# Optimization experiments

Measured on AMD Instinct MI355X. Metric: run time of the kernel, lower is better.

Reference implementation:

```python
import jax, jax.numpy as jnp
import numpy as np

C_IN = 64
C_QK = C_IN // 8  # 8
B, H, W = 8, 64, 64


def setup_inputs() -> dict:
    key = jax.random.key(0)
    ks = jax.random.split(key, 8)
    s_in = 1.0 / np.sqrt(C_IN)
    return {
        "x": jax.random.normal(ks[0], (B, C_IN, H, W), dtype=jnp.float32),
        "Wf": jax.random.normal(ks[1], (C_QK, C_IN), dtype=jnp.float32) * s_in,
        "bf": jax.random.normal(ks[2], (C_QK,), dtype=jnp.float32) * 0.01,
        "Wg": jax.random.normal(ks[3], (C_QK, C_IN), dtype=jnp.float32) * s_in,
        "bg": jax.random.normal(ks[4], (C_QK,), dtype=jnp.float32) * 0.01,
        "Wh": jax.random.normal(ks[5], (C_IN, C_IN), dtype=jnp.float32) * s_in,
        "bh": jax.random.normal(ks[6], (C_IN,), dtype=jnp.float32) * 0.01,
        "gamma": jax.random.normal(ks[7], (1,), dtype=jnp.float32) * 0.1,
    }


def reference(x, Wf, bf, Wg, bg, Wh, bh, gamma):
    Bn, C, Hn, Wn = x.shape
    N = Hn * Wn
    xf = x.reshape(Bn, C, N)  # (B, C, HW)
    # 1x1 convs == per-pixel linear projections
    fx = jnp.einsum('bcn,oc->bno', xf, Wf) + bf            # (B, HW, C/8)  (permuted query)
    gx = jnp.einsum('bcn,oc->bon', xf, Wg) + bg[:, None]   # (B, C/8, HW)
    hx = jnp.einsum('bcn,oc->bon', xf, Wh) + bh[:, None]   # (B, C,  HW)
    s_mtx = jnp.einsum('bno,bom->bnm', fx, gx)             # (B, HW, HW)
    attention = jax.nn.softmax(s_mtx, axis=-2)             # softmax over dim=-2 (rows)
    o = jnp.einsum('bcn,bnm->bcm', hx, attention)          # (B, C, HW)
    return x + gamma * o.reshape(Bn, C, Hn, Wn)
```

## Files before the change

### kernel.cpp

```cpp
#include <hip/hip_runtime.h>
#include <hip/hip_bf16.h>
#include <math.h>

#define CIN 64
#define CQK 8
#define BATCH 8
#define NPOS 4096
#define TN 128
#define NT (NPOS / TN)

typedef __attribute__((ext_vector_type(8))) short s16x8;
typedef __attribute__((ext_vector_type(4))) float f32x4;
typedef __attribute__((ext_vector_type(16))) float f32x16;

#define Z16 {0,0,0,0,0,0,0,0,0,0,0,0,0,0,0,0}

__device__ inline unsigned cvt_pk_bf16(float lo, float hi) {
    unsigned r;
    asm("v_cvt_pk_bf16_f32 %0, %1, %2" : "=v"(r) : "v"(lo), "v"(hi));
    return r;
}

__global__ __launch_bounds__(256) void proj_kernel(
    const float* __restrict__ x,
    const float* __restrict__ Wf, const float* __restrict__ bf,
    const float* __restrict__ Wg, const float* __restrict__ bg,
    const float* __restrict__ Wh, const float* __restrict__ bh,
    unsigned short* __restrict__ Kp, unsigned short* __restrict__ Qp,
    unsigned short* __restrict__ Vimg)
{
    __shared__ float xs[CIN * 66];
    __shared__ float bss[80];

    const int tid = threadIdx.x;
    const int b   = blockIdx.y;
    const int n0  = blockIdx.x * 64;

    if (tid < 80)
        bss[tid] = (tid < 8) ? bf[tid] : (tid < 16) ? bg[tid - 8] : bh[tid - 16];

    {
        const int c   = tid >> 2;
        const int seg = tid & 3;
        const float* src = x + ((size_t)(b * CIN + c)) * NPOS + n0 + seg * 16;
        float* dst = xs + c * 66 + seg * 16;
#pragma unroll
        for (int k = 0; k < 4; ++k) {
            const float4 v = *(const float4*)(src + k * 4);
            *(float2*)(dst + k * 4)     = make_float2(v.x, v.y);
            *(float2*)(dst + k * 4 + 2) = make_float2(v.z, v.w);
        }
    }

    const int l  = tid & 63;
    const int w  = tid >> 6;
    const int lm = l & 15;
    const int h  = l >> 4;

    auto wfrag = [&](const float* Wrow) -> s16x8 {
        const float4 a  = *(const float4*)(Wrow);
        const float4 bq = *(const float4*)(Wrow + 4);
        union { unsigned u[4]; s16x8 v; } r;
        r.u[0] = cvt_pk_bf16(a.x, a.y);
        r.u[1] = cvt_pk_bf16(a.z, a.w);
        r.u[2] = cvt_pk_bf16(bq.x, bq.y);
        r.u[3] = cvt_pk_bf16(bq.z, bq.w);
        return r.v;
    };

    const float* kqrow = (lm < 8) ? (Wf + lm * CIN) : (Wg + (lm - 8) * CIN);
    const s16x8 wkq0 = wfrag(kqrow + h * 8);
    const s16x8 wkq1 = wfrag(kqrow + h * 8 + 32);
    s16x8 wv0[4], wv1[4];
#pragma unroll
    for (int vt = 0; vt < 4; ++vt) {
        const float* vr = Wh + (vt * 16 + lm) * CIN + h * 8;
        wv0[vt] = wfrag(vr);
        wv1[vt] = wfrag(vr + 32);
    }

    __syncthreads();

    union { unsigned u[4]; s16x8 v; } xf0, xf1;
#pragma unroll
    for (int e2 = 0; e2 < 4; ++e2) {
        const int c = h * 8 + e2 * 2;
        xf0.u[e2] = cvt_pk_bf16(xs[c * 66 + w * 16 + lm],
                                xs[(c + 1) * 66 + w * 16 + lm]);
        xf1.u[e2] = cvt_pk_bf16(xs[(c + 32) * 66 + w * 16 + lm],
                                xs[(c + 33) * 66 + w * 16 + lm]);
    }

    const f32x4 z = {0.f, 0.f, 0.f, 0.f};
    f32x4 kq = __builtin_amdgcn_mfma_f32_16x16x32_bf16(wkq0, xf0.v, z, 0, 0, 0);
    kq = __builtin_amdgcn_mfma_f32_16x16x32_bf16(wkq1, xf1.v, kq, 0, 0, 0);
    f32x4 va[4];
#pragma unroll
    for (int vt = 0; vt < 4; ++vt) {
        va[vt] = __builtin_amdgcn_mfma_f32_16x16x32_bf16(xf0.v, wv0[vt], z, 0, 0, 0);
        va[vt] = __builtin_amdgcn_mfma_f32_16x16x32_bf16(xf1.v, wv1[vt], va[vt], 0, 0, 0);
    }

    const float LOG2E = 1.44269504088896f;

    {
        const int n = n0 + w * 16 + lm;
        float v0 = kq[0] + bss[h * 4 + 0];
        float v1 = kq[1] + bss[h * 4 + 1];
        float v2 = kq[2] + bss[h * 4 + 2];
        float v3 = kq[3] + bss[h * 4 + 3];
        if (h >= 2) { v0 *= LOG2E; v1 *= LOG2E; v2 *= LOG2E; v3 *= LOG2E; }
        uint2 pk;
        pk.x = cvt_pk_bf16(v0, v1);
        pk.y = cvt_pk_bf16(v2, v3);
        unsigned short* dstq =
            (h < 2 ? Kp : Qp) + ((size_t)(b * NPOS + n)) * CQK + (h & 1) * 4;
        *(uint2*)dstq = pk;
    }

    {
        const int t128 = n0 >> 7;
        const int sub  = ((n0 & 127) >> 5) + (w >> 1);
        unsigned short* dstB =
            Vimg + ((size_t)(b * 32 + t128)) * 8192 + (size_t)sub * 2048;
        const int jj   = (h & 1) * 2 + (w & 1);
        const int half = h >> 1;
#pragma unroll
        for (int vt = 0; vt < 4; ++vt) {
            const int C = vt * 16 + lm;
            const float bb = bss[16 + C];
            uint2 pk;
            pk.x = cvt_pk_bf16(va[vt][0] + bb, va[vt][1] + bb);
            pk.y = cvt_pk_bf16(va[vt][2] + bb, va[vt][3] + bb);
            const int p = ((jj & 1) * 2 + (C >> 5)) * 64 + (jj >> 1) * 32 + (C & 31);
            *(uint2*)(dstB + p * 8 + half * 4) = pk;
        }
    }
}

__global__ __launch_bounds__(256, 2) void attn_kernel(
    const unsigned short* __restrict__ Kp, const unsigned short* __restrict__ Qp,
    const unsigned short* __restrict__ Vimg, const float* __restrict__ x,
    const float* __restrict__ gamma, float* __restrict__ out)
{
    __shared__ __align__(16) float smem[4 * 64 * 36 + 256];
    float* reg = smem;
    float* rsl = smem + 4 * 64 * 36;

    const int tid = threadIdx.x;
    const int l   = tid & 63;
    const int w   = tid >> 6;
    const int lc  = l & 31;
    const int h   = l >> 5;
    const int id  = blockIdx.x;
    const int b   = id & 7;
    const int m0  = (id >> 3) * 64;

    const unsigned short* Kbat = Kp + (size_t)b * NPOS * CQK;
    const char* Vbat = (const char*)(Vimg + (size_t)b * NPOS * CIN);

    s16x8 qf0 = {0,0,0,0,0,0,0,0}, qf1 = {0,0,0,0,0,0,0,0};
    if (h == 0) {
        qf0 = *(const s16x8*)(Qp + ((size_t)(b * NPOS + m0 + lc)) * CQK);
        qf1 = *(const s16x8*)(Qp + ((size_t)(b * NPOS + m0 + 32 + lc)) * CQK);
    }

    f32x16 acc00 = Z16, acc01 = Z16, acc10 = Z16, acc11 = Z16;
    float rsum0 = 0.f, rsum1 = 0.f;

    s16x8 vfA[4], vfB[4], kaA, kaB;
    f32x16 scA0, scA1, scB0, scB1;
    const f32x16 z = Z16;

    auto loadV = [&](s16x8* vf, int t) {
        const char* base = Vbat + (size_t)t * 16384 + w * 4096 + l * 16;
#pragma unroll
        for (int c = 0; c < 4; ++c)
            vf[c] = *(const s16x8*)(base + c * 1024);
    };
    auto loadK = [&](s16x8& kr, int t) {
        kr = *(const s16x8*)(Kbat + ((size_t)(t * TN + w * 32 + lc)) * CQK);
    };

    auto proc = [&](f32x16& s0, f32x16& s1, const s16x8* vf) {
        __builtin_amdgcn_s_setprio(1);
#pragma unroll
        for (int rr = 0; rr < 16; ++rr) s0[rr] = __builtin_amdgcn_exp2f(s0[rr]);
        union { unsigned u[4]; s16x8 v; } A1, A2;
#pragma unroll
        for (int i = 0; i < 4; ++i) {
            A1.u[i] = cvt_pk_bf16(s0[2 * i], s0[2 * i + 1]);
            A2.u[i] = cvt_pk_bf16(s0[8 + 2 * i], s0[9 + 2 * i]);
        }
        rsum0 += (((s0[0] + s0[1]) + (s0[2] + s0[3])) +
                  ((s0[4] + s0[5]) + (s0[6] + s0[7]))) +
                 (((s0[8] + s0[9]) + (s0[10] + s0[11])) +
                  ((s0[12] + s0[13]) + (s0[14] + s0[15])));
        acc00 = __builtin_amdgcn_mfma_f32_32x32x16_bf16(A1.v, vf[0], acc00, 0, 0, 0);
        acc00 = __builtin_amdgcn_mfma_f32_32x32x16_bf16(A2.v, vf[2], acc00, 0, 0, 0);
        acc01 = __builtin_amdgcn_mfma_f32_32x32x16_bf16(A1.v, vf[1], acc01, 0, 0, 0);
        acc01 = __builtin_amdgcn_mfma_f32_32x32x16_bf16(A2.v, vf[3], acc01, 0, 0, 0);
#pragma unroll
        for (int rr = 0; rr < 16; ++rr) s1[rr] = __builtin_amdgcn_exp2f(s1[rr]);
        union { unsigned u[4]; s16x8 v; } B1, B2;
#pragma unroll
        for (int i = 0; i < 4; ++i) {
            B1.u[i] = cvt_pk_bf16(s1[2 * i], s1[2 * i + 1]);
            B2.u[i] = cvt_pk_bf16(s1[8 + 2 * i], s1[9 + 2 * i]);
        }
        rsum1 += (((s1[0] + s1[1]) + (s1[2] + s1[3])) +
                  ((s1[4] + s1[5]) + (s1[6] + s1[7]))) +
                 (((s1[8] + s1[9]) + (s1[10] + s1[11])) +
                  ((s1[12] + s1[13]) + (s1[14] + s1[15])));
        acc10 = __builtin_amdgcn_mfma_f32_32x32x16_bf16(B1.v, vf[0], acc10, 0, 0, 0);
        acc10 = __builtin_amdgcn_mfma_f32_32x32x16_bf16(B2.v, vf[2], acc10, 0, 0, 0);
        acc11 = __builtin_amdgcn_mfma_f32_32x32x16_bf16(B1.v, vf[1], acc11, 0, 0, 0);
        acc11 = __builtin_amdgcn_mfma_f32_32x32x16_bf16(B2.v, vf[3], acc11, 0, 0, 0);
        __builtin_amdgcn_s_setprio(0);
    };

    loadK(kaA, 0); loadV(vfA, 0);
    loadK(kaB, 1); loadV(vfB, 1);
    asm volatile("s_waitcnt vmcnt(5)" ::: "memory");
    scA0 = __builtin_amdgcn_mfma_f32_32x32x16_bf16(kaA, qf0, z, 0, 0, 0);
    scA1 = __builtin_amdgcn_mfma_f32_32x32x16_bf16(kaA, qf1, z, 0, 0, 0);

#pragma unroll 1
    for (int t = 0; t < NT - 2; t += 2) {
        asm volatile("s_waitcnt vmcnt(4)" ::: "memory");
        scB0 = __builtin_amdgcn_mfma_f32_32x32x16_bf16(kaB, qf0, z, 0, 0, 0);
        scB1 = __builtin_amdgcn_mfma_f32_32x32x16_bf16(kaB, qf1, z, 0, 0, 0);
        loadK(kaA, t + 2);
        proc(scA0, scA1, vfA);
        loadV(vfA, t + 2);
        asm volatile("s_waitcnt vmcnt(4)" ::: "memory");
        scA0 = __builtin_amdgcn_mfma_f32_32x32x16_bf16(kaA, qf0, z, 0, 0, 0);
        scA1 = __builtin_amdgcn_mfma_f32_32x32x16_bf16(kaA, qf1, z, 0, 0, 0);
        loadK(kaB, t + 3);
        proc(scB0, scB1, vfB);
        loadV(vfB, t + 3);
    }
    asm volatile("s_waitcnt vmcnt(4)" ::: "memory");
    scB0 = __builtin_amdgcn_mfma_f32_32x32x16_bf16(kaB, qf0, z, 0, 0, 0);
    scB1 = __builtin_amdgcn_mfma_f32_32x32x16_bf16(kaB, qf1, z, 0, 0, 0);
    proc(scA0, scA1, vfA);
    asm volatile("s_waitcnt vmcnt(0)" ::: "memory");
    proc(scB0, scB1, vfB);

    rsum0 += __shfl_xor(rsum0, 32, 64);
    rsum1 += __shfl_xor(rsum1, 32, 64);
    if (h == 0) {
        rsl[w * 64 + lc]      = rsum0;
        rsl[w * 64 + 32 + lc] = rsum1;
    }

    const float gm = gamma[0];
    auto epi = [&](const f32x16& a0, const f32x16& a1, int mOff) {
#pragma unroll
        for (int rq = 0; rq < 4; ++rq) {
            const int mb = 8 * rq + 4 * h;
            const f32x4 q0 = {a0[4 * rq], a0[4 * rq + 1], a0[4 * rq + 2], a0[4 * rq + 3]};
            const f32x4 q1 = {a1[4 * rq], a1[4 * rq + 1], a1[4 * rq + 2], a1[4 * rq + 3]};
            *(f32x4*)(reg + w * 2304 + lc * 36 + mb)        = q0;
            *(f32x4*)(reg + w * 2304 + (32 + lc) * 36 + mb) = q1;
        }
        __syncthreads();
        const int c  = tid >> 2;
        const int mq = tid & 3;
        const size_t base = ((size_t)(b * CIN + c)) * NPOS + m0 + mOff + mq * 8;
#pragma unroll
        for (int q4 = 0; q4 < 2; ++q4) {
            const float4 xv = *(const float4*)(x + base + q4 * 4);
            float4 o;
#pragma unroll
            for (int i = 0; i < 4; ++i) {
                const int ml = mq * 8 + q4 * 4 + i;
                const float rsum = (rsl[mOff + ml] + rsl[64 + mOff + ml]) +
                                   (rsl[128 + mOff + ml] + rsl[192 + mOff + ml]);
                const int oi = c * 36 + ml;
                const float os = (reg[oi] + reg[2304 + oi]) + (reg[4608 + oi] + reg[6912 + oi]);
                ((float*)&o)[i] = ((const float*)&xv)[i] + gm * os / rsum;
            }
            *(float4*)(out + base + q4 * 4) = o;
        }
        __syncthreads();
    };
    epi(acc00, acc01, 0);
    epi(acc10, acc11, 32);
}

extern "C" void kernel_launch(void* const* d_in, const int* in_sizes, int n_in,
                              void* d_out, int out_size, void* d_ws, size_t ws_size,
                              hipStream_t stream) {
    const float* x     = (const float*)d_in[0];
    const float* Wf    = (const float*)d_in[1];
    const float* bf    = (const float*)d_in[2];
    const float* Wg    = (const float*)d_in[3];
    const float* bg    = (const float*)d_in[4];
    const float* Wh    = (const float*)d_in[5];
    const float* bh    = (const float*)d_in[6];
    const float* gamma = (const float*)d_in[7];
    float* out = (float*)d_out;

    unsigned short* Kp = (unsigned short*)d_ws;
    unsigned short* Qp = Kp + (size_t)BATCH * NPOS * CQK;
    unsigned short* Vimg = Qp + (size_t)BATCH * NPOS * CQK;

    dim3 pgrid(NPOS / 64, BATCH);
    proj_kernel<<<pgrid, 256, 0, stream>>>(x, Wf, bf, Wg, bg, Wh, bh, Kp, Qp, Vimg);

    attn_kernel<<<dim3(BATCH * NPOS / 64), 256, 0, stream>>>(Kp, Qp, Vimg, x, gamma, out);
}
```

Before: 40.21 us.

## Split attention key range in two blocks and combine partials in new kernel

The attention kernel now splits the 4096 key positions into two halves handled by separate blocks, doubling the grid to 1024 blocks. Each block writes unnormalized partial outputs and row sums to workspace, and a new combine kernel sums the halves, normalizes, and adds the residual. The software pipeline is also restructured into a single-buffer score slot that interleaves the next QK MFMA with the current PV MFMAs, and occupancy is raised to 3 blocks per CU. This is meant to improve parallelism and latency hiding, at the cost of an extra kernel launch and extra global traffic for the partials (about 16 MB written and read).

Measured after the change: 56.98 us. +41.7%, slower.

```diff
diff --git a/kernel.cpp b/kernel.cpp
--- a/kernel.cpp
+++ b/kernel.cpp
@@ -7,7 +7,7 @@
 #define BATCH 8
 #define NPOS 4096
 #define TN 128
-#define NT (NPOS / TN)
+#define NT2 16
 
 typedef __attribute__((ext_vector_type(8))) short s16x8;
 typedef __attribute__((ext_vector_type(4))) float f32x4;
@@ -138,10 +138,10 @@
     }
 }
 
-__global__ __launch_bounds__(256, 2) void attn_kernel(
+__global__ __launch_bounds__(256, 3) void attn_kernel(
     const unsigned short* __restrict__ Kp, const unsigned short* __restrict__ Qp,
-    const unsigned short* __restrict__ Vimg, const float* __restrict__ x,
-    const float* __restrict__ gamma, float* __restrict__ out)
+    const unsigned short* __restrict__ Vimg,
+    float* __restrict__ Opart, float* __restrict__ Rpart)
 {
     __shared__ __align__(16) float smem[4 * 64 * 36 + 256];
     float* reg = smem;
@@ -154,7 +154,10 @@
     const int h   = l >> 5;
     const int id  = blockIdx.x;
     const int b   = id & 7;
-    const int m0  = (id >> 3) * 64;
+    const int nh  = (id >> 3) & 1;
+    const int m0  = (id >> 4) * 64;
+    const int t0  = nh * NT2;
+    const int tmax = t0 + NT2 - 1;
 
     const unsigned short* Kbat = Kp + (size_t)b * NPOS * CQK;
     const char* Vbat = (const char*)(Vimg + (size_t)b * NPOS * CIN);
@@ -168,8 +171,8 @@
     f32x16 acc00 = Z16, acc01 = Z16, acc10 = Z16, acc11 = Z16;
     float rsum0 = 0.f, rsum1 = 0.f;
 
-    s16x8 vfA[4], vfB[4], kaA, kaB;
-    f32x16 scA0, scA1, scB0, scB1;
+    s16x8 vfA[4], vfB[4], ka0, ka1;
+    f32x16 sc0, sc1;
     const f32x16 z = Z16;
 
     auto loadV = [&](s16x8* vf, int t) {
@@ -182,70 +185,67 @@
         kr = *(const s16x8*)(Kbat + ((size_t)(t * TN + w * 32 + lc)) * CQK);
     };
 
-    auto proc = [&](f32x16& s0, f32x16& s1, const s16x8* vf) {
+    auto slot = [&](s16x8* vfCur, const s16x8& kaUse, s16x8& kaLd,
+                    int t, int doNext) {
+        if (doNext) asm volatile("s_waitcnt vmcnt(4)" ::: "memory");
+        else        asm volatile("s_waitcnt vmcnt(0)" ::: "memory");
         __builtin_amdgcn_s_setprio(1);
 #pragma unroll
-        for (int rr = 0; rr < 16; ++rr) s0[rr] = __builtin_amdgcn_exp2f(s0[rr]);
-        union { unsigned u[4]; s16x8 v; } A1, A2;
+        for (int rr = 0; rr < 16; ++rr) {
+            sc0[rr] = __builtin_amdgcn_exp2f(sc0[rr]);
+            sc1[rr] = __builtin_amdgcn_exp2f(sc1[rr]);
+        }
+        union { unsigned u[4]; s16x8 v; } A1, A2, B1, B2;
 #pragma unroll
         for (int i = 0; i < 4; ++i) {
-            A1.u[i] = cvt_pk_bf16(s0[2 * i], s0[2 * i + 1]);
-            A2.u[i] = cvt_pk_bf16(s0[8 + 2 * i], s0[9 + 2 * i]);
-        }
-        rsum0 += (((s0[0] + s0[1]) + (s0[2] + s0[3])) +
-                  ((s0[4] + s0[5]) + (s0[6] + s0[7]))) +
-                 (((s0[8] + s0[9]) + (s0[10] + s0[11])) +
-                  ((s0[12] + s0[13]) + (s0[14] + s0[15])));
-        acc00 = __builtin_amdgcn_mfma_f32_32x32x16_bf16(A1.v, vf[0], acc00, 0, 0, 0);
-        acc00 = __builtin_amdgcn_mfma_f32_32x32x16_bf16(A2.v, vf[2], acc00, 0, 0, 0);
-        acc01 = __builtin_amdgcn_mfma_f32_32x32x16_bf16(A1.v, vf[1], acc01, 0, 0, 0);
-        acc01 = __builtin_amdgcn_mfma_f32_32x32x16_bf16(A2.v, vf[3], acc01, 0, 0, 0);
-#pragma unroll
-        for (int rr = 0; rr < 16; ++rr) s1[rr] = __builtin_amdgcn_exp2f(s1[rr]);
-        union { unsigned u[4]; s16x8 v; } B1, B2;
-#pragma unroll
-        for (int i = 0; i < 4; ++i) {
-            B1.u[i] = cvt_pk_bf16(s1[2 * i], s1[2 * i + 1]);
-            B2.u[i] = cvt_pk_bf16(s1[8 + 2 * i], s1[9 + 2 * i]);
-        }
-        rsum1 += (((s1[0] + s1[1]) + (s1[2] + s1[3])) +
-                  ((s1[4] + s1[5]) + (s1[6] + s1[7]))) +
-                 (((s1[8] + s1[9]) + (s1[10] + s1[11])) +
-                  ((s1[12] + s1[13]) + (s1[14] + s1[15])));
-        acc10 = __builtin_amdgcn_mfma_f32_32x32x16_bf16(B1.v, vf[0], acc10, 0, 0, 0);
-        acc10 = __builtin_amdgcn_mfma_f32_32x32x16_bf16(B2.v, vf[2], acc10, 0, 0, 0);
-        acc11 = __builtin_amdgcn_mfma_f32_32x32x16_bf16(B1.v, vf[1], acc11, 0, 0, 0);
-        acc11 = __builtin_amdgcn_mfma_f32_32x32x16_bf16(B2.v, vf[3], acc11, 0, 0, 0);
+            A1.u[i] = cvt_pk_bf16(sc0[2 * i], sc0[2 * i + 1]);
+            A2.u[i] = cvt_pk_bf16(sc0[8 + 2 * i], sc0[9 + 2 * i]);
+            B1.u[i] = cvt_pk_bf16(sc1[2 * i], sc1[2 * i + 1]);
+            B2.u[i] = cvt_pk_bf16(sc1[8 + 2 * i], sc1[9 + 2 * i]);
+        }
+        rsum0 += (((sc0[0] + sc0[1]) + (sc0[2] + sc0[3])) +
+                  ((sc0[4] + sc0[5]) + (sc0[6] + sc0[7]))) +
+                 (((sc0[8] + sc0[9]) + (sc0[10] + sc0[11])) +
+                  ((sc0[12] + sc0[13]) + (sc0[14] + sc0[15])));
+        rsum1 += (((sc1[0] + sc1[1]) + (sc1[2] + sc1[3])) +
+                  ((sc1[4] + sc1[5]) + (sc1[6] + sc1[7]))) +
+                 (((sc1[8] + sc1[9]) + (sc1[10] + sc1[11])) +
+                  ((sc1[12] + sc1[13]) + (sc1[14] + sc1[15])));
+        if (doNext) {
+            sc0 = __builtin_amdgcn_mfma_f32_32x32x16_bf16(kaUse, qf0, z, 0, 0, 0);
+            sc1 = __builtin_amdgcn_mfma_f32_32x32x16_bf16(kaUse, qf1, z, 0, 0, 0);
+            int tl = t + 2; if (tl > tmax) tl = tmax;
+            loadK(kaLd, tl);
+        }
+        acc00 = __builtin_amdgcn_mfma_f32_32x32x16_bf16(A1.v, vfCur[0], acc00, 0, 0, 0);
+        acc00 = __builtin_amdgcn_mfma_f32_32x32x16_bf16(A2.v, vfCur[2], acc00, 0, 0, 0);
+        acc01 = __builtin_amdgcn_mfma_f32_32x32x16_bf16(A1.v, vfCur[1], acc01, 0, 0, 0);
+        acc01 = __builtin_amdgcn_mfma_f32_32x32x16_bf16(A2.v, vfCur[3], acc01, 0, 0, 0);
+        acc10 = __builtin_amdgcn_mfma_f32_32x32x16_bf16(B1.v, vfCur[0], acc10, 0, 0, 0);
+        acc10 = __builtin_amdgcn_mfma_f32_32x32x16_bf16(B2.v, vfCur[2], acc10, 0, 0, 0);
+        acc11 = __builtin_amdgcn_mfma_f32_32x32x16_bf16(B1.v, vfCur[1], acc11, 0, 0, 0);
+        acc11 = __builtin_amdgcn_mfma_f32_32x32x16_bf16(B2.v, vfCur[3], acc11, 0, 0, 0);
         __builtin_amdgcn_s_setprio(0);
-    };
-
-    loadK(kaA, 0); loadV(vfA, 0);
-    loadK(kaB, 1); loadV(vfB, 1);
+        if (doNext) {
+            int tl = t + 2; if (tl > tmax) tl = tmax;
+            loadV(vfCur, tl);
+        }
+    };
+
+    loadK(ka0, t0);     loadV(vfA, t0);
+    loadK(ka1, t0 + 1); loadV(vfB, t0 + 1);
     asm volatile("s_waitcnt vmcnt(5)" ::: "memory");
-    scA0 = __builtin_amdgcn_mfma_f32_32x32x16_bf16(kaA, qf0, z, 0, 0, 0);
-    scA1 = __builtin_amdgcn_mfma_f32_32x32x16_bf16(kaA, qf1, z, 0, 0, 0);
-
+    sc0 = __builtin_amdgcn_mfma_f32_32x32x16_bf16(ka0, qf0, z, 0, 0, 0);
+    sc1 = __builtin_amdgcn_mfma_f32_32x32x16_bf16(ka0, qf1, z, 0, 0, 0);
+
+    slot(vfA, ka1, ka0, t0, 1);
 #pragma unroll 1
-    for (int t = 0; t < NT - 2; t += 2) {
-        asm volatile("s_waitcnt vmcnt(4)" ::: "memory");
-        scB0 = __builtin_amdgcn_mfma_f32_32x32x16_bf16(kaB, qf0, z, 0, 0, 0);
-        scB1 = __builtin_amdgcn_mfma_f32_32x32x16_bf16(kaB, qf1, z, 0, 0, 0);
-        loadK(kaA, t + 2);
-        proc(scA0, scA1, vfA);
-        loadV(vfA, t + 2);
-        asm volatile("s_waitcnt vmcnt(4)" ::: "memory");
-        scA0 = __builtin_amdgcn_mfma_f32_32x32x16_bf16(kaA, qf0, z, 0, 0, 0);
-        scA1 = __builtin_amdgcn_mfma_f32_32x32x16_bf16(kaA, qf1, z, 0, 0, 0);
-        loadK(kaB, t + 3);
-        proc(scB0, scB1, vfB);
-        loadV(vfB, t + 3);
-    }
-    asm volatile("s_waitcnt vmcnt(4)" ::: "memory");
-    scB0 = __builtin_amdgcn_mfma_f32_32x32x16_bf16(kaB, qf0, z, 0, 0, 0);
-    scB1 = __builtin_amdgcn_mfma_f32_32x32x16_bf16(kaB, qf1, z, 0, 0, 0);
-    proc(scA0, scA1, vfA);
-    asm volatile("s_waitcnt vmcnt(0)" ::: "memory");
-    proc(scB0, scB1, vfB);
+    for (int i = 0; i < 7; ++i) {
+        const int t = t0 + 1 + 2 * i;
+        slot(vfB, ka0, ka1, t, 1);
+        slot(vfA, ka1, ka0, t + 1, 1);
+    }
+    slot(vfB, ka0, ka1, tmax, 0);
 
     rsum0 += __shfl_xor(rsum0, 32, 64);
     rsum1 += __shfl_xor(rsum1, 32, 64);
@@ -254,7 +254,6 @@
         rsl[w * 64 + 32 + lc] = rsum1;
     }
 
-    const float gm = gamma[0];
     auto epi = [&](const f32x16& a0, const f32x16& a1, int mOff) {
 #pragma unroll
         for (int rq = 0; rq < 4; ++rq) {
@@ -267,26 +266,65 @@
         __syncthreads();
         const int c  = tid >> 2;
         const int mq = tid & 3;
-        const size_t base = ((size_t)(b * CIN + c)) * NPOS + m0 + mOff + mq * 8;
+        float* dst = Opart + ((size_t)id * 64 + c) * 64 + mOff + mq * 8;
 #pragma unroll
         for (int q4 = 0; q4 < 2; ++q4) {
-            const float4 xv = *(const float4*)(x + base + q4 * 4);
             float4 o;
 #pragma unroll
             for (int i = 0; i < 4; ++i) {
                 const int ml = mq * 8 + q4 * 4 + i;
-                const float rsum = (rsl[mOff + ml] + rsl[64 + mOff + ml]) +
-                                   (rsl[128 + mOff + ml] + rsl[192 + mOff + ml]);
                 const int oi = c * 36 + ml;
-                const float os = (reg[oi] + reg[2304 + oi]) + (reg[4608 + oi] + reg[6912 + oi]);
-                ((float*)&o)[i] = ((const float*)&xv)[i] + gm * os / rsum;
+                ((float*)&o)[i] = (reg[oi] + reg[2304 + oi]) +
+                                  (reg[4608 + oi] + reg[6912 + oi]);
             }
-            *(float4*)(out + base + q4 * 4) = o;
+            *(float4*)(dst + q4 * 4) = o;
         }
         __syncthreads();
     };
     epi(acc00, acc01, 0);
     epi(acc10, acc11, 32);
+
+    if (tid < 64)
+        Rpart[(size_t)id * 64 + tid] =
+            (rsl[tid] + rsl[64 + tid]) + (rsl[128 + tid] + rsl[192 + tid]);
+}
+
+__global__ __launch_bounds__(256) void comb_kernel(
+    const float* __restrict__ Opart, const float* __restrict__ Rpart,
+    const float* __restrict__ x, const float* __restrict__ gamma,
+    float* __restrict__ out)
+{
+    __shared__ float rs[64];
+    const int tid = threadIdx.x;
+    const int cid = blockIdx.x;
+    const int b   = cid & 7;
+    const int mg  = cid >> 3;
+    const int idA = b + mg * 16;
+    const int idB = idA + 8;
+
+    if (tid < 64)
+        rs[tid] = 1.0f / (Rpart[(size_t)idA * 64 + tid] +
+                          Rpart[(size_t)idB * 64 + tid]);
+    __syncthreads();
+
+    const float gm = gamma[0];
+    const int c  = tid >> 2;
+    const int m0 = (tid & 3) * 16;
+    const float* oA = Opart + ((size_t)idA * 64 + c) * 64 + m0;
+    const float* oB = Opart + ((size_t)idB * 64 + c) * 64 + m0;
+    const size_t base = ((size_t)(b * CIN + c)) * NPOS + mg * 64 + m0;
+#pragma unroll
+    for (int k = 0; k < 4; ++k) {
+        const float4 a  = *(const float4*)(oA + 4 * k);
+        const float4 bb = *(const float4*)(oB + 4 * k);
+        const float4 xv = *(const float4*)(x + base + 4 * k);
+        float4 r;
+        r.x = xv.x + gm * (a.x + bb.x) * rs[m0 + 4 * k + 0];
+        r.y = xv.y + gm * (a.y + bb.y) * rs[m0 + 4 * k + 1];
+        r.z = xv.z + gm * (a.z + bb.z) * rs[m0 + 4 * k + 2];
+        r.w = xv.w + gm * (a.w + bb.w) * rs[m0 + 4 * k + 3];
+        *(float4*)(out + base + 4 * k) = r;
+    }
 }
 
 extern "C" void kernel_launch(void* const* d_in, const int* in_sizes, int n_in,
@@ -302,12 +340,16 @@
     const float* gamma = (const float*)d_in[7];
     float* out = (float*)d_out;
 
-    unsigned short* Kp = (unsigned short*)d_ws;
-    unsigned short* Qp = Kp + (size_t)BATCH * NPOS * CQK;
+    unsigned short* Kp   = (unsigned short*)d_ws;
+    unsigned short* Qp   = Kp + (size_t)BATCH * NPOS * CQK;
     unsigned short* Vimg = Qp + (size_t)BATCH * NPOS * CQK;
+    float* Opart = (float*)(Vimg + (size_t)BATCH * NPOS * CIN);
+    float* Rpart = Opart + (size_t)1024 * 64 * 64;
 
     dim3 pgrid(NPOS / 64, BATCH);
     proj_kernel<<<pgrid, 256, 0, stream>>>(x, Wf, bf, Wg, bg, Wh, bh, Kp, Qp, Vimg);
 
-    attn_kernel<<<dim3(BATCH * NPOS / 64), 256, 0, stream>>>(Kp, Qp, Vimg, x, gamma, out);
-}
+    attn_kernel<<<dim3(1024), 256, 0, stream>>>(Kp, Qp, Vimg, Opart, Rpart);
+
+    comb_kernel<<<dim3(512), 256, 0, stream>>>(Opart, Rpart, x, gamma, out);
+}
```
